# Kernel tuning notes

Measured on AMD Instinct MI355X. Metric: run time of the kernel, lower is better.

The kernel has to match this reference:

```python
import jax, jax.numpy as jnp
import numpy as np

N = 50000        # nodes
E = 800000       # edges
F_IN = 16        # num_features
F_EDGE = 8       # num_edge_features
H = 4            # heads
C = 32           # hidden_dim (per-head out channels)
D = H * C        # 128, node state width
NUM_CLASSES = 5
NEG_SLOPE = 0.2  # PyG GATConv default leaky_relu slope


def setup_inputs() -> dict:
    key = jax.random.key(0)
    ks = jax.random.split(key, 30)
    def w(k, shape):
        return jax.random.normal(k, shape, dtype=jnp.float32) * 0.05
    return {
        "x": jax.random.normal(ks[0], (N, F_IN), dtype=jnp.float32),
        "edge_index": jax.random.randint(ks[1], (2, E), 0, N),
        "edge_attr": jax.random.normal(ks[2], (E, F_EDGE), dtype=jnp.float32),
        # edge_encoder: Linear(F_EDGE->C), ReLU, Linear(C->H)
        "ee_w1": w(ks[3], (C, F_EDGE)), "ee_b1": jnp.zeros((C,), jnp.float32),
        "ee_w2": w(ks[4], (H, C)),      "ee_b2": jnp.zeros((H,), jnp.float32),
        # input_proj: Linear(F_IN -> D)
        "proj_w": w(ks[5], (D, F_IN)), "proj_b": jnp.zeros((D,), jnp.float32),
        # conv1: GATConv(F_IN, C, heads=H, edge_dim=H, concat=True)
        "c1_lin": w(ks[6], (D, F_IN)),
        "c1_att_src": w(ks[7], (H, C)), "c1_att_dst": w(ks[8], (H, C)),
        "c1_lin_edge": w(ks[9], (D, H)), "c1_att_edge": w(ks[10], (H, C)),
        "c1_bias": jnp.zeros((D,), jnp.float32),
        # conv2: GATConv(D, C, heads=H, edge_dim=H, concat=True)
        "c2_lin": w(ks[11], (D, D)),
        "c2_att_src": w(ks[12], (H, C)), "c2_att_dst": w(ks[13], (H, C)),
        "c2_lin_edge": w(ks[14], (D, H)), "c2_att_edge": w(ks[15], (H, C)),
        "c2_bias": jnp.zeros((D,), jnp.float32),
        # layer norms
        "n1_g": jnp.ones((D,), jnp.float32), "n1_b": jnp.zeros((D,), jnp.float32),
        "n2_g": jnp.ones((D,), jnp.float32), "n2_b": jnp.zeros((D,), jnp.float32),
        # jk_proj: Linear(3D -> D)
        "jk_w": w(ks[16], (D, 3 * D)), "jk_b": jnp.zeros((D,), jnp.float32),
        # classifier: Linear(D -> NUM_CLASSES)
        "cls_w": w(ks[17], (NUM_CLASSES, D)), "cls_b": jnp.zeros((NUM_CLASSES,), jnp.float32),
    }


def _layer_norm(h, g, b, eps=1e-5):
    mu = jnp.mean(h, axis=-1, keepdims=True)
    var = jnp.var(h, axis=-1, keepdims=True)
    return (h - mu) * jax.lax.rsqrt(var + eps) * g + b


def _gat_conv(x, src, dst, e_attr, lin_w, att_src, att_dst, lin_edge_w, att_edge, bias):
    """PyG GATConv (v1) with edge features, concat=True, eval mode (no dropout)."""
    n = x.shape[0]
    xs = (x @ lin_w.T).reshape(n, H, C)                      # [N,H,C]
    a_src = jnp.einsum('nhc,hc->nh', xs, att_src)            # [N,H]
    a_dst = jnp.einsum('nhc,hc->nh', xs, att_dst)            # [N,H]
    ee = (e_attr @ lin_edge_w.T).reshape(-1, H, C)           # [E,H,C]
    a_edge = jnp.einsum('ehc,hc->eh', ee, att_edge)          # [E,H]
    alpha = jax.nn.leaky_relu(a_src[src] + a_dst[dst] + a_edge, NEG_SLOPE)
    # segment softmax over destination neighborhoods
    amax = jax.ops.segment_max(alpha, dst, num_segments=n)
    ex = jnp.exp(alpha - amax[dst])
    denom = jax.ops.segment_sum(ex, dst, num_segments=n)
    alpha = ex / (denom[dst] + 1e-16)                        # [E,H]
    msg = xs[src] * alpha[:, :, None]                        # [E,H,C]
    out = jax.ops.segment_sum(msg, dst, num_segments=n)      # [N,H,C]
    return out.reshape(n, H * C) + bias


def reference(x, edge_index, edge_attr,
              ee_w1, ee_b1, ee_w2, ee_b2,
              proj_w, proj_b,
              c1_lin, c1_att_src, c1_att_dst, c1_lin_edge, c1_att_edge, c1_bias,
              c2_lin, c2_att_src, c2_att_dst, c2_lin_edge, c2_att_edge, c2_bias,
              n1_g, n1_b, n2_g, n2_b,
              jk_w, jk_b, cls_w, cls_b):
    src, dst = edge_index[0], edge_index[1]
    # edge encoder
    e = jax.nn.relu(edge_attr @ ee_w1.T + ee_b1) @ ee_w2.T + ee_b2   # [E,H]
    h0 = x @ proj_w.T + proj_b                                        # [N,D]
    h1 = _gat_conv(x, src, dst, e, c1_lin, c1_att_src, c1_att_dst,
                   c1_lin_edge, c1_att_edge, c1_bias)
    h1 = _layer_norm(jax.nn.elu(h1) + h0, n1_g, n1_b)
    h2 = _gat_conv(h1, src, dst, e, c2_lin, c2_att_src, c2_att_dst,
                   c2_lin_edge, c2_att_edge, c2_bias)
    h2 = _layer_norm(jax.nn.elu(h2) + h1, n2_g, n2_b)
    h = jnp.concatenate([h0, h1, h2], axis=-1) @ jk_w.T + jk_b
    out = h @ cls_w.T + cls_b
    return jax.nn.log_softmax(out, axis=1)
```

## Files before the change

### kernel.cpp

```cpp
#include <hip/hip_runtime.h>
#include <cstdint>

#define NN 50000
#define NE 800000

using short8  = __attribute__((ext_vector_type(8))) short;
using float4v = __attribute__((ext_vector_type(4))) float;

__device__ __forceinline__ ushort f2bf(float f) {
    uint u = __float_as_uint(f);
    uint r = (u + 0x7fffu + ((u >> 16) & 1u)) >> 16;
    return (ushort)r;
}
__device__ __forceinline__ float bf2f(uint u) {
    return __uint_as_float(u << 16);
}

__global__ __launch_bounds__(256) void k_prep2(const float* __restrict__ le1, const float* __restrict__ ae1,
                                               const float* __restrict__ le2, const float* __restrict__ ae2,
                                               const float* __restrict__ jkw, const float* __restrict__ jkb,
                                               const float* __restrict__ clw, const float* __restrict__ clb,
                                               float* __restrict__ M, float* __restrict__ CW,
                                               float* __restrict__ cbp)
{
    int idx = blockIdx.x * 256 + threadIdx.x;
    if (idx < 32) {
        const float* le = (idx < 16) ? le1 : le2;
        const float* ae = (idx < 16) ? ae1 : ae2;
        int hk = idx & 15, h = hk >> 2, k = hk & 3;
        float s = 0.f;
        for (int c = 0; c < 32; ++c)
            s += le[(h * 32 + c) * 4 + k] * ae[h * 32 + c];
        M[idx] = s;
    } else if (idx < 32 + 1920) {
        int o = idx - 32;
        int r = o / 384, c = o - r * 384;
        float s = 0.f;
        for (int k = 0; k < 128; ++k)
            s += clw[r * 128 + k] * jkw[(size_t)k * 384 + c];
        CW[o] = s;
    } else if (idx < 32 + 1920 + 5) {
        int r = idx - 1952;
        float s = clb[r];
        for (int k = 0; k < 128; ++k)
            s += clw[r * 128 + k] * jkb[k];
        cbp[r] = s;
    }
}

__global__ void k_zero_int(int* __restrict__ p, int cnt)
{
    int i = blockIdx.x * 256 + threadIdx.x;
    if (i < cnt) p[i] = 0;
}

__global__ __launch_bounds__(256) void k_hist(const int* __restrict__ ei, int* __restrict__ deg)
{
    int e = blockIdx.x * 256 + threadIdx.x;
    if (e < NE) atomicAdd(&deg[ei[NE + e]], 1);
}

__global__ __launch_bounds__(256) void k_scan_blk(const int* __restrict__ deg,
                                                  int* __restrict__ loc,
                                                  int* __restrict__ bsum)
{
    __shared__ int tmp[256];
    int t = threadIdx.x;
    int i = blockIdx.x * 256 + t;
    int v = (i < NN) ? deg[i] : 0;
    tmp[t] = v;
    __syncthreads();
    #pragma unroll
    for (int o = 1; o < 256; o <<= 1) {
        int add = (t >= o) ? tmp[t - o] : 0;
        __syncthreads();
        tmp[t] += add;
        __syncthreads();
    }
    if (i < NN) loc[i] = tmp[t] - v;
    if (t == 255) bsum[blockIdx.x] = tmp[255];
}

__global__ __launch_bounds__(256) void k_scan_top(const int* __restrict__ bsum,
                                                  int* __restrict__ bcarry,
                                                  int* __restrict__ total_out, int nb)
{
    __shared__ int tmp[256];
    int t = threadIdx.x;
    int v = (t < nb) ? bsum[t] : 0;
    tmp[t] = v;
    __syncthreads();
    #pragma unroll
    for (int o = 1; o < 256; o <<= 1) {
        int add = (t >= o) ? tmp[t - o] : 0;
        __syncthreads();
        tmp[t] += add;
        __syncthreads();
    }
    if (t < nb) bcarry[t] = tmp[t] - v;
    if (t == 255) *total_out = tmp[255];
}

__global__ __launch_bounds__(256) void k_scan_add(const int* __restrict__ loc,
                                                  const int* __restrict__ bcarry,
                                                  int* __restrict__ off,
                                                  int* __restrict__ cur)
{
    int i = blockIdx.x * 256 + threadIdx.x;
    if (i < NN) {
        int o = loc[i] + bcarry[blockIdx.x];
        off[i] = o;
        cur[i] = o;
    }
}

__global__ __launch_bounds__(256) void k_edge_scatter(const float* __restrict__ ea,
                                                      const float* __restrict__ w1,
                                                      const float* __restrict__ b1,
                                                      const float* __restrict__ w2,
                                                      const float* __restrict__ b2,
                                                      const int* __restrict__ ei,
                                                      int* __restrict__ cursor,
                                                      int* __restrict__ csrs,
                                                      float4* __restrict__ e4c)
{
    __shared__ float sw1[256], sb1[32], sw2[128], sb2[4];
    int t = threadIdx.x;
    sw1[t] = w1[t];
    if (t < 128) sw2[t] = w2[t];
    if (t < 32)  sb1[t] = b1[t];
    if (t < 4)   sb2[t] = b2[t];
    __syncthreads();
    int e = blockIdx.x * 256 + t;
    if (e >= NE) return;
    float4 x0 = *(const float4*)(ea + (size_t)e * 8);
    float4 x1 = *(const float4*)(ea + (size_t)e * 8 + 4);
    float o0 = sb2[0], o1 = sb2[1], o2 = sb2[2], o3 = sb2[3];
    #pragma unroll
    for (int j = 0; j < 32; ++j) {
        const float* w = sw1 + j * 8;
        float s = sb1[j] + w[0]*x0.x + w[1]*x0.y + w[2]*x0.z + w[3]*x0.w
                         + w[4]*x1.x + w[5]*x1.y + w[6]*x1.z + w[7]*x1.w;
        s = fmaxf(s, 0.f);
        o0 += sw2[0*32+j] * s; o1 += sw2[1*32+j] * s;
        o2 += sw2[2*32+j] * s; o3 += sw2[3*32+j] * s;
    }
    int src = ei[e], dst = ei[NE + e];
    int p = atomicAdd(&cursor[dst], 1);
    csrs[p] = src;
    e4c[p] = make_float4(o0, o1, o2, o3);
}

__global__ __launch_bounds__(256) void k_cvt_pad(const float* __restrict__ src,
                                                 ushort* __restrict__ dst,
                                                 int rows, int ks, int kd)
{
    int i = blockIdx.x * 256 + threadIdx.x;
    if (i >= rows * kd) return;
    int r = i / kd, c = i - r * kd;
    dst[i] = (c < ks) ? f2bf(src[(size_t)r * ks + c]) : (ushort)0;
}

__global__ __launch_bounds__(256) void gemm_bf16(const ushort* __restrict__ A, int lda, int K,
                                                 const ushort* __restrict__ W, int ldw,
                                                 const float* __restrict__ bias,
                                                 ushort* __restrict__ Cb, int ldcb, int M)
{
    int t = threadIdx.x;
    int wv = t >> 6, lane = t & 63;
    int quad = lane >> 4, r16 = lane & 15;
    int m0 = blockIdx.x * 128 + wv * 32;
    float4v acc[2][8];
    #pragma unroll
    for (int i = 0; i < 2; ++i)
        #pragma unroll
        for (int j = 0; j < 8; ++j) acc[i][j] = (float4v){0.f, 0.f, 0.f, 0.f};
    int ar0 = m0 + r16;      if (ar0 >= M) ar0 = M - 1;
    int ar1 = m0 + 16 + r16; if (ar1 >= M) ar1 = M - 1;
    const ushort* a0p = A + (size_t)ar0 * lda + quad * 8;
    const ushort* a1p = A + (size_t)ar1 * lda + quad * 8;
    const ushort* wp  = W + (size_t)r16 * ldw + quad * 8;
    for (int k0 = 0; k0 < K; k0 += 32) {
        short8 a0 = *(const short8*)(a0p + k0);
        short8 a1 = *(const short8*)(a1p + k0);
        #pragma unroll
        for (int nt = 0; nt < 8; ++nt) {
            short8 b = *(const short8*)(wp + (size_t)(nt * 16) * ldw + k0);
            acc[0][nt] = __builtin_amdgcn_mfma_f32_16x16x32_bf16(a0, b, acc[0][nt], 0, 0, 0);
            acc[1][nt] = __builtin_amdgcn_mfma_f32_16x16x32_bf16(a1, b, acc[1][nt], 0, 0, 0);
        }
    }
    #pragma unroll
    for (int rt = 0; rt < 2; ++rt) {
        #pragma unroll
        for (int nt = 0; nt < 8; ++nt) {
            int col = nt * 16 + r16;
            float bv = bias ? bias[col] : 0.f;
            #pragma unroll
            for (int r = 0; r < 4; ++r) {
                int row = m0 + rt * 16 + quad * 4 + r;
                if (row < M)
                    Cb[(size_t)row * ldcb + col] = f2bf(acc[rt][nt][r] + bv);
            }
        }
    }
}

__global__ __launch_bounds__(256) void k_att_reduce(const ushort* __restrict__ xs,
                                                    const float* __restrict__ att_src,
                                                    const float* __restrict__ att_dst,
                                                    float* __restrict__ as_out,
                                                    float* __restrict__ ad_out)
{
    __shared__ float ssrc[128], sdst[128];
    int t = threadIdx.x;
    if (t < 128) { ssrc[t] = att_src[t]; sdst[t] = att_dst[t]; }
    __syncthreads();
    int n = blockIdx.x * 256 + t;
    if (n >= NN) return;
    float s[4] = {0,0,0,0}, d[4] = {0,0,0,0};
    const uint2* xr = (const uint2*)(xs + (size_t)n * 128);
    #pragma unroll
    for (int q = 0; q < 32; ++q) {
        uint2 p = xr[q];
        float v0 = bf2f(p.x & 0xffffu), v1 = bf2f(p.x >> 16);
        float v2 = bf2f(p.y & 0xffffu), v3 = bf2f(p.y >> 16);
        int h = q >> 3;
        const float* aw = ssrc + q * 4;
        const float* dw = sdst + q * 4;
        s[h] += v0*aw[0] + v1*aw[1] + v2*aw[2] + v3*aw[3];
        d[h] += v0*dw[0] + v1*dw[1] + v2*dw[2] + v3*dw[3];
    }
    *(float4*)(as_out + (size_t)n * 4) = make_float4(s[0], s[1], s[2], s[3]);
    *(float4*)(ad_out + (size_t)n * 4) = make_float4(d[0], d[1], d[2], d[3]);
}

__global__ __launch_bounds__(256) void k_agg2(const int* __restrict__ off,
                                              const int* __restrict__ csrs,
                                              const float4* __restrict__ e4c,
                                              const float* __restrict__ as_in,
                                              const float* __restrict__ ad_in,
                                              const float* __restrict__ Mm,
                                              const ushort* __restrict__ xs,
                                              const float* __restrict__ bias,
                                              const ushort* __restrict__ residb,
                                              const float* __restrict__ g,
                                              const float* __restrict__ bln,
                                              ushort* __restrict__ outb)
{
    int wave = threadIdx.x >> 6;
    int lane = threadIdx.x & 63;
    int n = blockIdx.x * 4 + wave;
    if (n >= NN) return;
    int i0 = off[n], i1 = off[n + 1];
    int c0 = lane * 2;
    int h = lane >> 4;
    float m0 = Mm[h*4+0], m1 = Mm[h*4+1], m2 = Mm[h*4+2], m3 = Mm[h*4+3];
    float adh = ad_in[(size_t)n * 4 + h];
    float a0 = 0.f, a1 = 0.f, den = 0.f;
    int i = i0;
    for (; i + 4 <= i1; i += 4) {
        int s0 = csrs[i], s1 = csrs[i+1], s2 = csrs[i+2], s3 = csrs[i+3];
        float4 e0 = e4c[i], e1 = e4c[i+1], e2 = e4c[i+2], e3 = e4c[i+3];
        float y0 = as_in[(size_t)s0*4+h], y1 = as_in[(size_t)s1*4+h];
        float y2 = as_in[(size_t)s2*4+h], y3 = as_in[(size_t)s3*4+h];
        uint p0 = *(const uint*)(xs + (size_t)s0*128 + c0);
        uint p1 = *(const uint*)(xs + (size_t)s1*128 + c0);
        uint p2 = *(const uint*)(xs + (size_t)s2*128 + c0);
        uint p3 = *(const uint*)(xs + (size_t)s3*128 + c0);
        float al0 = y0 + adh + m0*e0.x + m1*e0.y + m2*e0.z + m3*e0.w;
        float al1 = y1 + adh + m0*e1.x + m1*e1.y + m2*e1.z + m3*e1.w;
        float al2 = y2 + adh + m0*e2.x + m1*e2.y + m2*e2.z + m3*e2.w;
        float al3 = y3 + adh + m0*e3.x + m1*e3.y + m2*e3.z + m3*e3.w;
        al0 = al0 > 0.f ? al0 : 0.2f*al0;
        al1 = al1 > 0.f ? al1 : 0.2f*al1;
        al2 = al2 > 0.f ? al2 : 0.2f*al2;
        al3 = al3 > 0.f ? al3 : 0.2f*al3;
        float w0 = __expf(al0), w1 = __expf(al1), w2 = __expf(al2), w3 = __expf(al3);
        a0 = fmaf(bf2f(p0 & 0xffffu), w0, a0); a1 = fmaf(bf2f(p0 >> 16), w0, a1);
        a0 = fmaf(bf2f(p1 & 0xffffu), w1, a0); a1 = fmaf(bf2f(p1 >> 16), w1, a1);
        a0 = fmaf(bf2f(p2 & 0xffffu), w2, a0); a1 = fmaf(bf2f(p2 >> 16), w2, a1);
        a0 = fmaf(bf2f(p3 & 0xffffu), w3, a0); a1 = fmaf(bf2f(p3 >> 16), w3, a1);
        den += (w0 + w1) + (w2 + w3);
    }
    for (; i < i1; ++i) {
        int s0 = csrs[i];
        float4 e0 = e4c[i];
        float y0 = as_in[(size_t)s0*4+h];
        uint p0 = *(const uint*)(xs + (size_t)s0*128 + c0);
        float al0 = y0 + adh + m0*e0.x + m1*e0.y + m2*e0.z + m3*e0.w;
        al0 = al0 > 0.f ? al0 : 0.2f*al0;
        float w0 = __expf(al0);
        a0 = fmaf(bf2f(p0 & 0xffffu), w0, a0);
        a1 = fmaf(bf2f(p0 >> 16), w0, a1);
        den += w0;
    }
    float inv = 1.f / (den + 1e-16f);
    float v0 = a0 * inv + bias[c0];
    float v1 = a1 * inv + bias[c0 + 1];
    v0 = v0 > 0.f ? v0 : (__expf(v0) - 1.f);
    v1 = v1 > 0.f ? v1 : (__expf(v1) - 1.f);
    uint rp = *(const uint*)(residb + (size_t)n * 384 + c0);
    float r0 = v0 + bf2f(rp & 0xffffu);
    float r1 = v1 + bf2f(rp >> 16);
    float ssum = r0 + r1, ssq = r0 * r0 + r1 * r1;
    #pragma unroll
    for (int o = 1; o < 64; o <<= 1) {
        ssum += __shfl_xor(ssum, o, 64);
        ssq  += __shfl_xor(ssq, o, 64);
    }
    float mu = ssum * (1.f / 128.f);
    float var = ssq * (1.f / 128.f) - mu * mu;
    float rs = rsqrtf(var + 1e-5f);
    float o0 = (r0 - mu) * rs * g[c0] + bln[c0];
    float o1 = (r1 - mu) * rs * g[c0 + 1] + bln[c0 + 1];
    uint pk = (uint)f2bf(o0) | ((uint)f2bf(o1) << 16);
    *(uint*)(outb + (size_t)n * 384 + c0) = pk;
}

__global__ __launch_bounds__(256) void k_cls(const ushort* __restrict__ hcatb,
                                             const float* __restrict__ CW,
                                             const float* __restrict__ cbp,
                                             float* __restrict__ out)
{
    __shared__ float sCW[1920], scb[5];
    int t = threadIdx.x;
    for (int i = t; i < 1920; i += 256) sCW[i] = CW[i];
    if (t < 5) scb[t] = cbp[t];
    __syncthreads();
    int n = blockIdx.x * 256 + t;
    if (n >= NN) return;
    float acc[5] = {scb[0], scb[1], scb[2], scb[3], scb[4]};
    const uint2* hr = (const uint2*)(hcatb + (size_t)n * 384);
    #pragma unroll 4
    for (int q = 0; q < 96; ++q) {
        uint2 p = hr[q];
        float v0 = bf2f(p.x & 0xffffu), v1 = bf2f(p.x >> 16);
        float v2 = bf2f(p.y & 0xffffu), v3 = bf2f(p.y >> 16);
        #pragma unroll
        for (int o = 0; o < 5; ++o) {
            const float* w = sCW + o * 384 + q * 4;
            acc[o] += v0*w[0] + v1*w[1] + v2*w[2] + v3*w[3];
        }
    }
    float m = acc[0];
    #pragma unroll
    for (int o = 1; o < 5; ++o) m = fmaxf(m, acc[o]);
    float sum = 0.f;
    #pragma unroll
    for (int o = 0; o < 5; ++o) sum += __expf(acc[o] - m);
    float lse = __logf(sum) + m;
    float* op = out + (size_t)n * 5;
    #pragma unroll
    for (int o = 0; o < 5; ++o) op[o] = acc[o] - lse;
}

extern "C" void kernel_launch(void* const* d_in, const int* in_sizes, int n_in,
                              void* d_out, int out_size, void* d_ws, size_t ws_size,
                              hipStream_t stream)
{
    (void)in_sizes; (void)n_in; (void)out_size; (void)ws_size;
    const float* x        = (const float*)d_in[0];
    const int*   ei       = (const int*)d_in[1];
    const float* eattr    = (const float*)d_in[2];
    const float* ee_w1    = (const float*)d_in[3];
    const float* ee_b1    = (const float*)d_in[4];
    const float* ee_w2    = (const float*)d_in[5];
    const float* ee_b2    = (const float*)d_in[6];
    const float* proj_w   = (const float*)d_in[7];
    const float* proj_b   = (const float*)d_in[8];
    const float* c1_lin   = (const float*)d_in[9];
    const float* c1_asrc  = (const float*)d_in[10];
    const float* c1_adst  = (const float*)d_in[11];
    const float* c1_ledge = (const float*)d_in[12];
    const float* c1_aedge = (const float*)d_in[13];
    const float* c1_bias  = (const float*)d_in[14];
    const float* c2_lin   = (const float*)d_in[15];
    const float* c2_asrc  = (const float*)d_in[16];
    const float* c2_adst  = (const float*)d_in[17];
    const float* c2_ledge = (const float*)d_in[18];
    const float* c2_aedge = (const float*)d_in[19];
    const float* c2_bias  = (const float*)d_in[20];
    const float* n1_g     = (const float*)d_in[21];
    const float* n1_b     = (const float*)d_in[22];
    const float* n2_g     = (const float*)d_in[23];
    const float* n2_b     = (const float*)d_in[24];
    const float* jk_w     = (const float*)d_in[25];
    const float* jk_b     = (const float*)d_in[26];
    const float* cls_w    = (const float*)d_in[27];
    const float* cls_b    = (const float*)d_in[28];
    float* out = (float*)d_out;
    float* ws  = (float*)d_ws;

    const size_t oM   = 0;
    const size_t oCW  = 64;
    const size_t oCB  = oCW + 1920;
    const size_t oE4C = 2048;
    const size_t oHB  = oE4C + (size_t)NE * 4;
    const size_t oXS  = oHB + (size_t)NN * 192;
    const size_t oXP  = oXS + (size_t)NN * 64;
    const size_t oWB  = oXP + (size_t)NN * 16;
    const size_t oAS  = oWB + 12288;
    const size_t oAD  = oAS + (size_t)NN * 4;
    const size_t oI   = oAD + (size_t)NN * 4;

    float*  Mmat  = ws + oM;
    float*  CW    = ws + oCW;
    float*  cbp   = ws + oCB;
    float4* e4c   = (float4*)(ws + oE4C);
    ushort* hcatb = (ushort*)(ws + oHB);
    ushort* xs    = (ushort*)(ws + oXS);
    ushort* xpad  = (ushort*)(ws + oXP);
    ushort* wb    = (ushort*)(ws + oWB);
    ushort* pwb   = wb;
    ushort* c1b   = wb + 4096;
    ushort* c2b   = wb + 8192;
    float*  as_b  = ws + oAS;
    float*  ad_b  = ws + oAD;
    int*    ip    = (int*)(ws + oI);
    int*    deg   = ip;
    int*    loc   = ip + NN;
    int*    off   = ip + 2 * NN;
    int*    cur   = ip + 3 * NN + 16;
    int*    bsum  = ip + 4 * NN + 16;
    int*    bcar  = ip + 4 * NN + 272;
    int*    csrs  = ip + 4 * NN + 528;

    const int EB  = (NE + 255) / 256;
    const int NB  = (NN + 255) / 256;
    const int GB  = (NN + 127) / 128;
    const int WB2 = (NN + 3) / 4;

    k_zero_int<<<NB, 256, 0, stream>>>(deg, NN);
    k_hist<<<EB, 256, 0, stream>>>(ei, deg);
    k_scan_blk<<<NB, 256, 0, stream>>>(deg, loc, bsum);
    k_scan_top<<<1, 256, 0, stream>>>(bsum, bcar, off + NN, NB);
    k_scan_add<<<NB, 256, 0, stream>>>(loc, bcar, off, cur);

    k_prep2<<<8, 256, 0, stream>>>(c1_ledge, c1_aedge, c2_ledge, c2_aedge,
                                   jk_w, jk_b, cls_w, cls_b, Mmat, CW, cbp);
    k_edge_scatter<<<EB, 256, 0, stream>>>(eattr, ee_w1, ee_b1, ee_w2, ee_b2,
                                           ei, cur, csrs, e4c);

    k_cvt_pad<<<(NN*32 + 255)/256, 256, 0, stream>>>(x, xpad, NN, 16, 32);
    k_cvt_pad<<<16, 256, 0, stream>>>(proj_w, pwb, 128, 16, 32);
    k_cvt_pad<<<16, 256, 0, stream>>>(c1_lin, c1b, 128, 16, 32);
    k_cvt_pad<<<64, 256, 0, stream>>>(c2_lin, c2b, 128, 128, 128);

    gemm_bf16<<<GB, 256, 0, stream>>>(xpad, 32, 32, pwb, 32, proj_b, hcatb, 384, NN);
    gemm_bf16<<<GB, 256, 0, stream>>>(xpad, 32, 32, c1b, 32, nullptr, xs, 128, NN);

    k_att_reduce<<<NB, 256, 0, stream>>>(xs, c1_asrc, c1_adst, as_b, ad_b);
    k_agg2<<<WB2, 256, 0, stream>>>(off, csrs, e4c, as_b, ad_b, Mmat,
                                    xs, c1_bias, hcatb, n1_g, n1_b, hcatb + 128);

    gemm_bf16<<<GB, 256, 0, stream>>>(hcatb + 128, 384, 128, c2b, 128, nullptr, xs, 128, NN);
    k_att_reduce<<<NB, 256, 0, stream>>>(xs, c2_asrc, c2_adst, as_b, ad_b);
    k_agg2<<<WB2, 256, 0, stream>>>(off, csrs, e4c, as_b, ad_b, Mmat + 16,
                                    xs, c2_bias, hcatb + 128, n2_g, n2_b, hcatb + 256);

    k_cls<<<NB, 256, 0, stream>>>(hcatb, CW, cbp, out);
}
```

Before: 427.5 us.

## Fuse edge MLP with histogram, store edge ids in CSR, fuse first GEMMs

Folds the degree histogram into the edge-encoder kernel and writes edge features in original edge order. A lightweight scatter kernel then stores (src, edge id) pairs in the CSR, so aggregation gathers edge features indirectly instead of reading them in CSR order. The input projection and the conv1 linear are fused into one MFMA kernel that converts x to bf16 on the fly. Weight conversions are merged into the prep kernel, which removes several small launches and the padded-x buffer. The cost is random gathers of edge features in both aggregation passes instead of contiguous reads.

After: 418.9 us. 2.0% less time.

```diff
diff --git a/kernel.cpp b/kernel.cpp
--- a/kernel.cpp
+++ b/kernel.cpp
@@ -20,8 +20,11 @@
                                                const float* __restrict__ le2, const float* __restrict__ ae2,
                                                const float* __restrict__ jkw, const float* __restrict__ jkb,
                                                const float* __restrict__ clw, const float* __restrict__ clb,
+                                               const float* __restrict__ projw, const float* __restrict__ c1lin,
+                                               const float* __restrict__ c2lin,
                                                float* __restrict__ M, float* __restrict__ CW,
-                                               float* __restrict__ cbp)
+                                               float* __restrict__ cbp,
+                                               ushort* __restrict__ w01b, ushort* __restrict__ c2b)
 {
     int idx = blockIdx.x * 256 + threadIdx.x;
     if (idx < 32) {
@@ -32,19 +35,28 @@
         for (int c = 0; c < 32; ++c)
             s += le[(h * 32 + c) * 4 + k] * ae[h * 32 + c];
         M[idx] = s;
-    } else if (idx < 32 + 1920) {
+    } else if (idx < 1952) {
         int o = idx - 32;
         int r = o / 384, c = o - r * 384;
         float s = 0.f;
         for (int k = 0; k < 128; ++k)
             s += clw[r * 128 + k] * jkw[(size_t)k * 384 + c];
         CW[o] = s;
-    } else if (idx < 32 + 1920 + 5) {
+    } else if (idx < 1957) {
         int r = idx - 1952;
         float s = clb[r];
         for (int k = 0; k < 128; ++k)
             s += clw[r * 128 + k] * jkb[k];
         cbp[r] = s;
+    } else if (idx >= 2048 && idx < 10240) {
+        int o = idx - 2048;
+        int r = o >> 5, c = o & 31;
+        float v = 0.f;
+        if (c < 16) v = (r < 128) ? projw[r * 16 + c] : c1lin[(r - 128) * 16 + c];
+        w01b[o] = f2bf(v);
+    } else if (idx >= 10240 && idx < 26624) {
+        int o = idx - 10240;
+        c2b[o] = f2bf(c2lin[o]);
     }
 }
 
@@ -54,75 +66,14 @@
     if (i < cnt) p[i] = 0;
 }
 
-__global__ __launch_bounds__(256) void k_hist(const int* __restrict__ ei, int* __restrict__ deg)
-{
-    int e = blockIdx.x * 256 + threadIdx.x;
-    if (e < NE) atomicAdd(&deg[ei[NE + e]], 1);
-}
-
-__global__ __launch_bounds__(256) void k_scan_blk(const int* __restrict__ deg,
-                                                  int* __restrict__ loc,
-                                                  int* __restrict__ bsum)
-{
-    __shared__ int tmp[256];
-    int t = threadIdx.x;
-    int i = blockIdx.x * 256 + t;
-    int v = (i < NN) ? deg[i] : 0;
-    tmp[t] = v;
-    __syncthreads();
-    #pragma unroll
-    for (int o = 1; o < 256; o <<= 1) {
-        int add = (t >= o) ? tmp[t - o] : 0;
-        __syncthreads();
-        tmp[t] += add;
-        __syncthreads();
-    }
-    if (i < NN) loc[i] = tmp[t] - v;
-    if (t == 255) bsum[blockIdx.x] = tmp[255];
-}
-
-__global__ __launch_bounds__(256) void k_scan_top(const int* __restrict__ bsum,
-                                                  int* __restrict__ bcarry,
-                                                  int* __restrict__ total_out, int nb)
-{
-    __shared__ int tmp[256];
-    int t = threadIdx.x;
-    int v = (t < nb) ? bsum[t] : 0;
-    tmp[t] = v;
-    __syncthreads();
-    #pragma unroll
-    for (int o = 1; o < 256; o <<= 1) {
-        int add = (t >= o) ? tmp[t - o] : 0;
-        __syncthreads();
-        tmp[t] += add;
-        __syncthreads();
-    }
-    if (t < nb) bcarry[t] = tmp[t] - v;
-    if (t == 255) *total_out = tmp[255];
-}
-
-__global__ __launch_bounds__(256) void k_scan_add(const int* __restrict__ loc,
-                                                  const int* __restrict__ bcarry,
-                                                  int* __restrict__ off,
-                                                  int* __restrict__ cur)
-{
-    int i = blockIdx.x * 256 + threadIdx.x;
-    if (i < NN) {
-        int o = loc[i] + bcarry[blockIdx.x];
-        off[i] = o;
-        cur[i] = o;
-    }
-}
-
-__global__ __launch_bounds__(256) void k_edge_scatter(const float* __restrict__ ea,
-                                                      const float* __restrict__ w1,
-                                                      const float* __restrict__ b1,
-                                                      const float* __restrict__ w2,
-                                                      const float* __restrict__ b2,
-                                                      const int* __restrict__ ei,
-                                                      int* __restrict__ cursor,
-                                                      int* __restrict__ csrs,
-                                                      float4* __restrict__ e4c)
+__global__ __launch_bounds__(256) void k_edge_mlp(const float* __restrict__ ea,
+                                                  const float* __restrict__ w1,
+                                                  const float* __restrict__ b1,
+                                                  const float* __restrict__ w2,
+                                                  const float* __restrict__ b2,
+                                                  const int* __restrict__ ei,
+                                                  int* __restrict__ deg,
+                                                  float4* __restrict__ e4out)
 {
     __shared__ float sw1[256], sb1[32], sw2[128], sb2[4];
     int t = threadIdx.x;
@@ -145,25 +96,130 @@
         o0 += sw2[0*32+j] * s; o1 += sw2[1*32+j] * s;
         o2 += sw2[2*32+j] * s; o3 += sw2[3*32+j] * s;
     }
+    e4out[e] = make_float4(o0, o1, o2, o3);
+    atomicAdd(&deg[ei[NE + e]], 1);
+}
+
+__global__ __launch_bounds__(256) void k_scan_blk(const int* __restrict__ deg,
+                                                  int* __restrict__ loc,
+                                                  int* __restrict__ bsum)
+{
+    __shared__ int tmp[256];
+    int t = threadIdx.x;
+    int i = blockIdx.x * 256 + t;
+    int v = (i < NN) ? deg[i] : 0;
+    tmp[t] = v;
+    __syncthreads();
+    #pragma unroll
+    for (int o = 1; o < 256; o <<= 1) {
+        int add = (t >= o) ? tmp[t - o] : 0;
+        __syncthreads();
+        tmp[t] += add;
+        __syncthreads();
+    }
+    if (i < NN) loc[i] = tmp[t] - v;
+    if (t == 255) bsum[blockIdx.x] = tmp[255];
+}
+
+__global__ __launch_bounds__(256) void k_scan_top(const int* __restrict__ bsum,
+                                                  int* __restrict__ bcarry,
+                                                  int* __restrict__ total_out, int nb)
+{
+    __shared__ int tmp[256];
+    int t = threadIdx.x;
+    int v = (t < nb) ? bsum[t] : 0;
+    tmp[t] = v;
+    __syncthreads();
+    #pragma unroll
+    for (int o = 1; o < 256; o <<= 1) {
+        int add = (t >= o) ? tmp[t - o] : 0;
+        __syncthreads();
+        tmp[t] += add;
+        __syncthreads();
+    }
+    if (t < nb) bcarry[t] = tmp[t] - v;
+    if (t == 255) *total_out = tmp[255];
+}
+
+__global__ __launch_bounds__(256) void k_scan_add(const int* __restrict__ loc,
+                                                  const int* __restrict__ bcarry,
+                                                  int* __restrict__ off,
+                                                  int* __restrict__ cur)
+{
+    int i = blockIdx.x * 256 + threadIdx.x;
+    if (i < NN) {
+        int o = loc[i] + bcarry[blockIdx.x];
+        off[i] = o;
+        cur[i] = o;
+    }
+}
+
+__global__ __launch_bounds__(256) void k_scatter2(const int* __restrict__ ei,
+                                                  int* __restrict__ cursor,
+                                                  int2* __restrict__ csr2)
+{
+    int e = blockIdx.x * 256 + threadIdx.x;
+    if (e >= NE) return;
     int src = ei[e], dst = ei[NE + e];
     int p = atomicAdd(&cursor[dst], 1);
-    csrs[p] = src;
-    e4c[p] = make_float4(o0, o1, o2, o3);
-}
-
-__global__ __launch_bounds__(256) void k_cvt_pad(const float* __restrict__ src,
-                                                 ushort* __restrict__ dst,
-                                                 int rows, int ks, int kd)
-{
-    int i = blockIdx.x * 256 + threadIdx.x;
-    if (i >= rows * kd) return;
-    int r = i / kd, c = i - r * kd;
-    dst[i] = (c < ks) ? f2bf(src[(size_t)r * ks + c]) : (ushort)0;
+    csr2[p] = make_int2(src, e);
+}
+
+__global__ __launch_bounds__(256) void k_gemm1(const float* __restrict__ x,
+                                               const ushort* __restrict__ w01,
+                                               const float* __restrict__ pbias,
+                                               ushort* __restrict__ hcatb,
+                                               ushort* __restrict__ xs, int M)
+{
+    int t = threadIdx.x;
+    int wv = t >> 6, lane = t & 63;
+    int quad = lane >> 4, r16 = lane & 15;
+    int m0 = blockIdx.x * 128 + wv * 32;
+    int ar0 = m0 + r16;      if (ar0 >= M) ar0 = M - 1;
+    int ar1 = m0 + 16 + r16; if (ar1 >= M) ar1 = M - 1;
+    short8 a0 = (short8){0,0,0,0,0,0,0,0}, a1 = a0;
+    if (quad < 2) {
+        const float* p0 = x + (size_t)ar0 * 16 + quad * 8;
+        const float* p1 = x + (size_t)ar1 * 16 + quad * 8;
+        float4 u0 = *(const float4*)p0, u1 = *(const float4*)(p0 + 4);
+        float4 v0 = *(const float4*)p1, v1 = *(const float4*)(p1 + 4);
+        a0[0]=(short)f2bf(u0.x); a0[1]=(short)f2bf(u0.y); a0[2]=(short)f2bf(u0.z); a0[3]=(short)f2bf(u0.w);
+        a0[4]=(short)f2bf(u1.x); a0[5]=(short)f2bf(u1.y); a0[6]=(short)f2bf(u1.z); a0[7]=(short)f2bf(u1.w);
+        a1[0]=(short)f2bf(v0.x); a1[1]=(short)f2bf(v0.y); a1[2]=(short)f2bf(v0.z); a1[3]=(short)f2bf(v0.w);
+        a1[4]=(short)f2bf(v1.x); a1[5]=(short)f2bf(v1.y); a1[6]=(short)f2bf(v1.z); a1[7]=(short)f2bf(v1.w);
+    }
+    float4v acc[2][16];
+    #pragma unroll
+    for (int i = 0; i < 2; ++i)
+        #pragma unroll
+        for (int j = 0; j < 16; ++j) acc[i][j] = (float4v){0.f, 0.f, 0.f, 0.f};
+    #pragma unroll
+    for (int nt = 0; nt < 16; ++nt) {
+        short8 b = *(const short8*)(w01 + (size_t)(nt * 16 + r16) * 32 + quad * 8);
+        acc[0][nt] = __builtin_amdgcn_mfma_f32_16x16x32_bf16(a0, b, acc[0][nt], 0, 0, 0);
+        acc[1][nt] = __builtin_amdgcn_mfma_f32_16x16x32_bf16(a1, b, acc[1][nt], 0, 0, 0);
+    }
+    #pragma unroll
+    for (int rt = 0; rt < 2; ++rt) {
+        #pragma unroll
+        for (int nt = 0; nt < 16; ++nt) {
+            int col = (nt & 7) * 16 + r16;
+            float bv = (nt < 8) ? pbias[col] : 0.f;
+            #pragma unroll
+            for (int r = 0; r < 4; ++r) {
+                int row = m0 + rt * 16 + quad * 4 + r;
+                if (row < M) {
+                    float v = acc[rt][nt][r] + bv;
+                    if (nt < 8) hcatb[(size_t)row * 384 + col] = f2bf(v);
+                    else        xs[(size_t)row * 128 + col] = f2bf(v);
+                }
+            }
+        }
+    }
 }
 
 __global__ __launch_bounds__(256) void gemm_bf16(const ushort* __restrict__ A, int lda, int K,
                                                  const ushort* __restrict__ W, int ldw,
-                                                 const float* __restrict__ bias,
                                                  ushort* __restrict__ Cb, int ldcb, int M)
 {
     int t = threadIdx.x;
@@ -195,12 +251,11 @@
         #pragma unroll
         for (int nt = 0; nt < 8; ++nt) {
             int col = nt * 16 + r16;
-            float bv = bias ? bias[col] : 0.f;
             #pragma unroll
             for (int r = 0; r < 4; ++r) {
                 int row = m0 + rt * 16 + quad * 4 + r;
                 if (row < M)
-                    Cb[(size_t)row * ldcb + col] = f2bf(acc[rt][nt][r] + bv);
+                    Cb[(size_t)row * ldcb + col] = f2bf(acc[rt][nt][r]);
             }
         }
     }
@@ -236,8 +291,8 @@
 }
 
 __global__ __launch_bounds__(256) void k_agg2(const int* __restrict__ off,
-                                              const int* __restrict__ csrs,
-                                              const float4* __restrict__ e4c,
+                                              const int2* __restrict__ csr2,
+                                              const float4* __restrict__ e4g,
                                               const float* __restrict__ as_in,
                                               const float* __restrict__ ad_in,
                                               const float* __restrict__ Mm,
@@ -260,14 +315,14 @@
     float a0 = 0.f, a1 = 0.f, den = 0.f;
     int i = i0;
     for (; i + 4 <= i1; i += 4) {
-        int s0 = csrs[i], s1 = csrs[i+1], s2 = csrs[i+2], s3 = csrs[i+3];
-        float4 e0 = e4c[i], e1 = e4c[i+1], e2 = e4c[i+2], e3 = e4c[i+3];
-        float y0 = as_in[(size_t)s0*4+h], y1 = as_in[(size_t)s1*4+h];
-        float y2 = as_in[(size_t)s2*4+h], y3 = as_in[(size_t)s3*4+h];
-        uint p0 = *(const uint*)(xs + (size_t)s0*128 + c0);
-        uint p1 = *(const uint*)(xs + (size_t)s1*128 + c0);
-        uint p2 = *(const uint*)(xs + (size_t)s2*128 + c0);
-        uint p3 = *(const uint*)(xs + (size_t)s3*128 + c0);
+        int2 se0 = csr2[i], se1 = csr2[i+1], se2 = csr2[i+2], se3 = csr2[i+3];
+        float4 e0 = e4g[se0.y], e1 = e4g[se1.y], e2 = e4g[se2.y], e3 = e4g[se3.y];
+        float y0 = as_in[(size_t)se0.x*4+h], y1 = as_in[(size_t)se1.x*4+h];
+        float y2 = as_in[(size_t)se2.x*4+h], y3 = as_in[(size_t)se3.x*4+h];
+        uint p0 = *(const uint*)(xs + (size_t)se0.x*128 + c0);
+        uint p1 = *(const uint*)(xs + (size_t)se1.x*128 + c0);
+        uint p2 = *(const uint*)(xs + (size_t)se2.x*128 + c0);
+        uint p3 = *(const uint*)(xs + (size_t)se3.x*128 + c0);
         float al0 = y0 + adh + m0*e0.x + m1*e0.y + m2*e0.z + m3*e0.w;
         float al1 = y1 + adh + m0*e1.x + m1*e1.y + m2*e1.z + m3*e1.w;
         float al2 = y2 + adh + m0*e2.x + m1*e2.y + m2*e2.z + m3*e2.w;
@@ -284,10 +339,10 @@
         den += (w0 + w1) + (w2 + w3);
     }
     for (; i < i1; ++i) {
-        int s0 = csrs[i];
-        float4 e0 = e4c[i];
-        float y0 = as_in[(size_t)s0*4+h];
-        uint p0 = *(const uint*)(xs + (size_t)s0*128 + c0);
+        int2 se0 = csr2[i];
+        float4 e0 = e4g[se0.y];
+        float y0 = as_in[(size_t)se0.x*4+h];
+        uint p0 = *(const uint*)(xs + (size_t)se0.x*128 + c0);
         float al0 = y0 + adh + m0*e0.x + m1*e0.y + m2*e0.z + m3*e0.w;
         al0 = al0 > 0.f ? al0 : 0.2f*al0;
         float w0 = __expf(al0);
@@ -395,11 +450,10 @@
     const size_t oM   = 0;
     const size_t oCW  = 64;
     const size_t oCB  = oCW + 1920;
-    const size_t oE4C = 2048;
-    const size_t oHB  = oE4C + (size_t)NE * 4;
+    const size_t oE4  = 2048;
+    const size_t oHB  = oE4 + (size_t)NE * 4;
     const size_t oXS  = oHB + (size_t)NN * 192;
-    const size_t oXP  = oXS + (size_t)NN * 64;
-    const size_t oWB  = oXP + (size_t)NN * 16;
+    const size_t oWB  = oXS + (size_t)NN * 64;
     const size_t oAS  = oWB + 12288;
     const size_t oAD  = oAS + (size_t)NN * 4;
     const size_t oI   = oAD + (size_t)NN * 4;
@@ -407,14 +461,11 @@
     float*  Mmat  = ws + oM;
     float*  CW    = ws + oCW;
     float*  cbp   = ws + oCB;
-    float4* e4c   = (float4*)(ws + oE4C);
+    float4* e4g   = (float4*)(ws + oE4);
     ushort* hcatb = (ushort*)(ws + oHB);
     ushort* xs    = (ushort*)(ws + oXS);
-    ushort* xpad  = (ushort*)(ws + oXP);
-    ushort* wb    = (ushort*)(ws + oWB);
-    ushort* pwb   = wb;
-    ushort* c1b   = wb + 4096;
-    ushort* c2b   = wb + 8192;
+    ushort* w01b  = (ushort*)(ws + oWB);
+    ushort* c2b   = w01b + 8192;
     float*  as_b  = ws + oAS;
     float*  ad_b  = ws + oAD;
     int*    ip    = (int*)(ws + oI);
@@ -424,7 +475,7 @@
     int*    cur   = ip + 3 * NN + 16;
     int*    bsum  = ip + 4 * NN + 16;
     int*    bcar  = ip + 4 * NN + 272;
-    int*    csrs  = ip + 4 * NN + 528;
+    int2*   csr2  = (int2*)(ip + 4 * NN + 528);
 
     const int EB  = (NE + 255) / 256;
     const int NB  = (NN + 255) / 256;
@@ -432,31 +483,25 @@
     const int WB2 = (NN + 3) / 4;
 
     k_zero_int<<<NB, 256, 0, stream>>>(deg, NN);
-    k_hist<<<EB, 256, 0, stream>>>(ei, deg);
+    k_prep2<<<104, 256, 0, stream>>>(c1_ledge, c1_aedge, c2_ledge, c2_aedge,
+                                     jk_w, jk_b, cls_w, cls_b,
+                                     proj_w, c1_lin, c2_lin,
+                                     Mmat, CW, cbp, w01b, c2b);
+    k_edge_mlp<<<EB, 256, 0, stream>>>(eattr, ee_w1, ee_b1, ee_w2, ee_b2, ei, deg, e4g);
     k_scan_blk<<<NB, 256, 0, stream>>>(deg, loc, bsum);
     k_scan_top<<<1, 256, 0, stream>>>(bsum, bcar, off + NN, NB);
     k_scan_add<<<NB, 256, 0, stream>>>(loc, bcar, off, cur);
-
-    k_prep2<<<8, 256, 0, stream>>>(c1_ledge, c1_aedge, c2_ledge, c2_aedge,
-                                   jk_w, jk_b, cls_w, cls_b, Mmat, CW, cbp);
-    k_edge_scatter<<<EB, 256, 0, stream>>>(eattr, ee_w1, ee_b1, ee_w2, ee_b2,
-                                           ei, cur, csrs, e4c);
-
-    k_cvt_pad<<<(NN*32 + 255)/256, 256, 0, stream>>>(x, xpad, NN, 16, 32);
-    k_cvt_pad<<<16, 256, 0, stream>>>(proj_w, pwb, 128, 16, 32);
-    k_cvt_pad<<<16, 256, 0, stream>>>(c1_lin, c1b, 128, 16, 32);
-    k_cvt_pad<<<64, 256, 0, stream>>>(c2_lin, c2b, 128, 128, 128);
-
-    gemm_bf16<<<GB, 256, 0, stream>>>(xpad, 32, 32, pwb, 32, proj_b, hcatb, 384, NN);
-    gemm_bf16<<<GB, 256, 0, stream>>>(xpad, 32, 32, c1b, 32, nullptr, xs, 128, NN);
+    k_scatter2<<<EB, 256, 0, stream>>>(ei, cur, csr2);
+
+    k_gemm1<<<GB, 256, 0, stream>>>(x, w01b, proj_b, hcatb, xs, NN);
 
     k_att_reduce<<<NB, 256, 0, stream>>>(xs, c1_asrc, c1_adst, as_b, ad_b);
-    k_agg2<<<WB2, 256, 0, stream>>>(off, csrs, e4c, as_b, ad_b, Mmat,
+    k_agg2<<<WB2, 256, 0, stream>>>(off, csr2, e4g, as_b, ad_b, Mmat,
                                     xs, c1_bias, hcatb, n1_g, n1_b, hcatb + 128);
 
-    gemm_bf16<<<GB, 256, 0, stream>>>(hcatb + 128, 384, 128, c2b, 128, nullptr, xs, 128, NN);
+    gemm_bf16<<<GB, 256, 0, stream>>>(hcatb + 128, 384, 128, c2b, 128, xs, 128, NN);
     k_att_reduce<<<NB, 256, 0, stream>>>(xs, c2_asrc, c2_adst, as_b, ad_b);
-    k_agg2<<<WB2, 256, 0, stream>>>(off, csrs, e4c, as_b, ad_b, Mmat + 16,
+    k_agg2<<<WB2, 256, 0, stream>>>(off, csr2, e4g, as_b, ad_b, Mmat + 16,
                                     xs, c2_bias, hcatb + 128, n2_g, n2_b, hcatb + 256);
 
     k_cls<<<NB, 256, 0, stream>>>(hcatb, CW, cbp, out);
```
